# Performance work log

Measured on AMD Instinct MI355X. Metric: run time of the kernel, lower is better.

## Reference

```python
import jax, jax.numpy as jnp
import numpy as np

NEG_INF = -1e9


def setup_inputs() -> dict:
    key = jax.random.key(0)
    k1, k2, k3, k4 = jax.random.split(key, 4)
    B, S, D, P = 4, 256, 512, 256
    sequence = jax.random.normal(k1, (B, S, D), dtype=jnp.float32)
    sequence_mask = jnp.ones((B, S), dtype=jnp.float32)
    W1 = jax.random.normal(k2, (P, D), dtype=jnp.float32) * (1.0 / np.sqrt(D))
    W2 = jax.random.normal(k3, (P, D), dtype=jnp.float32) * (1.0 / np.sqrt(D))
    v = jax.random.normal(k4, (P,), dtype=jnp.float32) * (1.0 / np.sqrt(P))
    return {"sequence": sequence, "sequence_mask": sequence_mask,
            "W1": W1, "W2": W2, "v": v}


def reference(sequence, sequence_mask, W1, W2, v):
    # sequence: [B, S, D]; sequence_mask: [B, S] (1 = valid)
    # Projection (additive) self-attention, vectorized over all query positions.
    pk = jnp.einsum('bsd,pd->bsp', sequence, W1)  # key projections  [B, S, P]
    pq = jnp.einsum('bsd,pd->bsp', sequence, W2)  # query projections [B, S, P]
    # scores[b, i, j] = v . tanh(pq[b, i] + pk[b, j])   (i = query, j = key)
    scores = jnp.einsum('bijp,p->bij',
                        jnp.tanh(pq[:, :, None, :] + pk[:, None, :, :]), v)
    # mask keys, softmax over key dim
    key_mask = sequence_mask[:, None, :] > 0          # [B, 1, S]
    scores = jnp.where(key_mask, scores, NEG_INF)
    weights = jax.nn.softmax(scores, axis=-1)         # [B, Sq, Sk]
    attn = jnp.einsum('bij,bjd->bid', weights, sequence)  # [B, S, D]
    # mask_sequence: zero out invalid query positions
    attn = attn * sequence_mask[:, :, None]
    weights = weights * sequence_mask[:, :, None]
    return attn, weights
```

## Files before the change

kernel.cpp:

```cpp
#include <hip/hip_runtime.h>

constexpr int B = 4;
constexpr int S = 256;
constexpr int D = 512;
constexpr int P = 256;
constexpr float NEG_INF = -1e9f;
constexpr float LOG2E = 1.4426950408889634f;
constexpr float C2 = 2.885390081777927f;

__device__ __forceinline__ float fast_exp2(float x) {
#if __has_builtin(__builtin_amdgcn_exp2f)
    return __builtin_amdgcn_exp2f(x);
#else
    return exp2f(x);
#endif
}

__device__ __forceinline__ float fast_rcp(float x) {
#if __has_builtin(__builtin_amdgcn_rcpf)
    return __builtin_amdgcn_rcpf(x);
#else
    return 1.0f / x;
#endif
}

__global__ __launch_bounds__(256)
void proj_kernel(const float* __restrict__ seq,
                 const float* __restrict__ W1, const float* __restrict__ W2,
                 float* __restrict__ pq, float* __restrict__ pkT) {
    __shared__ float As[64][34];
    __shared__ float Ws[64][68];

    int bid0 = blockIdx.x;
    int bid = (bid0 & 7) * 32 + (bid0 >> 3);

    const float* A;
    const float* Bp;
    float* out;
    if (bid < 128) {
        int mt = bid >> 2, nt = bid & 3;
        A = seq + (size_t)mt * 32 * D;
        Bp = W2 + (size_t)nt * 64 * D;
        out = pq + (size_t)mt * 32 * 256 + nt * 64;
    } else {
        int r = bid - 128;
        int b = r >> 5, t = r & 31;
        int mt = t >> 2, nt = t & 3;
        A = W1 + (size_t)mt * 32 * D;
        Bp = seq + ((size_t)b * S + nt * 64) * D;
        out = pkT + (size_t)b * P * S + (size_t)mt * 32 * 256 + nt * 64;
    }

    int tid = threadIdx.x;
    int tx = tid & 15, ty = tid >> 4;
    int ar = tid >> 3, acg = tid & 7;
    int br = tid >> 2, bcg = tid & 3;
    const float* aptr = A + (size_t)ar * D + acg * 8;
    const float* bptr = Bp + (size_t)br * D + bcg * 16;

    float4 a0, a1, w0, w1, w2, w3;
    a0 = *(const float4*)(aptr);      a1 = *(const float4*)(aptr + 4);
    w0 = *(const float4*)(bptr);      w1 = *(const float4*)(bptr + 4);
    w2 = *(const float4*)(bptr + 8);  w3 = *(const float4*)(bptr + 12);

    float c0[4] = {0.f, 0.f, 0.f, 0.f};
    float c1[4] = {0.f, 0.f, 0.f, 0.f};

    for (int kt = 0; kt < 8; kt++) {
        int ka = acg * 8;
        As[ka + 0][ar] = a0.x; As[ka + 1][ar] = a0.y;
        As[ka + 2][ar] = a0.z; As[ka + 3][ar] = a0.w;
        As[ka + 4][ar] = a1.x; As[ka + 5][ar] = a1.y;
        As[ka + 6][ar] = a1.z; As[ka + 7][ar] = a1.w;
        int kb = bcg * 16;
        Ws[kb + 0][br] = w0.x;  Ws[kb + 1][br] = w0.y;
        Ws[kb + 2][br] = w0.z;  Ws[kb + 3][br] = w0.w;
        Ws[kb + 4][br] = w1.x;  Ws[kb + 5][br] = w1.y;
        Ws[kb + 6][br] = w1.z;  Ws[kb + 7][br] = w1.w;
        Ws[kb + 8][br] = w2.x;  Ws[kb + 9][br] = w2.y;
        Ws[kb + 10][br] = w2.z; Ws[kb + 11][br] = w2.w;
        Ws[kb + 12][br] = w3.x; Ws[kb + 13][br] = w3.y;
        Ws[kb + 14][br] = w3.z; Ws[kb + 15][br] = w3.w;
        __syncthreads();
        if (kt < 7) {
            const float* ap = aptr + (kt + 1) * 64;
            const float* bp = bptr + (kt + 1) * 64;
            a0 = *(const float4*)(ap);     a1 = *(const float4*)(ap + 4);
            w0 = *(const float4*)(bp);     w1 = *(const float4*)(bp + 4);
            w2 = *(const float4*)(bp + 8); w3 = *(const float4*)(bp + 12);
        }
#pragma unroll 8
        for (int k = 0; k < 64; k++) {
            float2 av = *(const float2*)&As[k][ty * 2];
            float4 wv = *(const float4*)&Ws[k][tx * 4];
            c0[0] = fmaf(av.x, wv.x, c0[0]);
            c0[1] = fmaf(av.x, wv.y, c0[1]);
            c0[2] = fmaf(av.x, wv.z, c0[2]);
            c0[3] = fmaf(av.x, wv.w, c0[3]);
            c1[0] = fmaf(av.y, wv.x, c1[0]);
            c1[1] = fmaf(av.y, wv.y, c1[1]);
            c1[2] = fmaf(av.y, wv.z, c1[2]);
            c1[3] = fmaf(av.y, wv.w, c1[3]);
        }
        __syncthreads();
    }
    float4 o0 = {c0[0] * C2, c0[1] * C2, c0[2] * C2, c0[3] * C2};
    float4 o1 = {c1[0] * C2, c1[1] * C2, c1[2] * C2, c1[3] * C2};
    *(float4*)&out[(size_t)(ty * 2 + 0) * 256 + tx * 4] = o0;
    *(float4*)&out[(size_t)(ty * 2 + 1) * 256 + tx * 4] = o1;
}

__global__ __launch_bounds__(512)
void score_attn_kernel(const float* __restrict__ seq,
                       const float* __restrict__ pkT, const float* __restrict__ pq,
                       const float* __restrict__ v, const float* __restrict__ mask,
                       float* __restrict__ wout, float* __restrict__ attn) {
    __shared__ float pqs[2][P];
    __shared__ float vs[P];
    __shared__ float part[4][2][S];
    __shared__ float wsm[S][2];
    __shared__ float p3[4][2][D];
    __shared__ float redm[2][8], reds[2][8];

    int bid0 = blockIdx.x;
    int bid = (bid0 & 7) * 64 + (bid0 >> 3);
    int b = bid >> 7;
    int i0 = (bid & 127) * 2;
    int tid = threadIdx.x;
    int lane = tid & 63, wid = tid >> 6;

    if (tid < 256) {
        ((float2*)pqs)[tid] = ((const float2*)(pq + ((size_t)b * S + i0) * P))[tid];
    } else if (tid < 384) {
        int x = tid - 256;
        float2 vv = ((const float2*)v)[x];
        ((float2*)vs)[x] = make_float2(-2.f * vv.x, -2.f * vv.y);
    }
    __syncthreads();

    {
        int jg = tid & 127, h = tid >> 7;
        const float2* kp = (const float2*)(pkT + (size_t)b * P * S);
        float acc00 = 0.f, acc01 = 0.f, acc10 = 0.f, acc11 = 0.f;
        int pbase = h * 64;
#pragma unroll 4
        for (int pp = 0; pp < 64; pp += 4) {
            int p = pbase + pp;
            float2 k0 = kp[(size_t)(p + 0) * 128 + jg];
            float2 k1 = kp[(size_t)(p + 1) * 128 + jg];
            float2 k2 = kp[(size_t)(p + 2) * 128 + jg];
            float2 k3 = kp[(size_t)(p + 3) * 128 + jg];
            float4 vv = *(const float4*)&vs[p];
            float4 q0 = *(const float4*)&pqs[0][p];
            float4 q1 = *(const float4*)&pqs[1][p];
#define TANH4(kv, vvv, qa, qb)                                     \
            {                                                      \
                float t00 = fast_exp2(kv.x + qa);                  \
                float t01 = fast_exp2(kv.y + qa);                  \
                float t10 = fast_exp2(kv.x + qb);                  \
                float t11 = fast_exp2(kv.y + qb);                  \
                acc00 = fmaf(vvv, fast_rcp(t00 + 1.f), acc00);     \
                acc01 = fmaf(vvv, fast_rcp(t01 + 1.f), acc01);     \
                acc10 = fmaf(vvv, fast_rcp(t10 + 1.f), acc10);     \
                acc11 = fmaf(vvv, fast_rcp(t11 + 1.f), acc11);     \
            }
            TANH4(k0, vv.x, q0.x, q1.x)
            TANH4(k1, vv.y, q0.y, q1.y)
            TANH4(k2, vv.z, q0.z, q1.z)
            TANH4(k3, vv.w, q0.w, q1.w)
#undef TANH4
        }
        int j0 = 2 * jg;
        part[h][0][j0] = acc00; part[h][0][j0 + 1] = acc01;
        part[h][1][j0] = acc10; part[h][1][j0 + 1] = acc11;
    }
    __syncthreads();

    float s0 = -3.0e38f, s1 = -3.0e38f;
    if (tid < 256) {
        int j = tid;
        s0 = (part[0][0][j] + part[1][0][j]) + (part[2][0][j] + part[3][0][j]);
        s1 = (part[0][1][j] + part[1][1][j]) + (part[2][1][j] + part[3][1][j]);
        float km = mask[(size_t)b * S + j];
        if (!(km > 0.f)) { s0 = NEG_INF; s1 = NEG_INF; }
    }
    float m0 = s0, m1 = s1;
#pragma unroll
    for (int off = 32; off >= 1; off >>= 1) {
        m0 = fmaxf(m0, __shfl_xor(m0, off, 64));
        m1 = fmaxf(m1, __shfl_xor(m1, off, 64));
    }
    if (lane == 0) { redm[0][wid] = m0; redm[1][wid] = m1; }
    __syncthreads();
    m0 = fmaxf(fmaxf(redm[0][0], redm[0][1]), fmaxf(redm[0][2], redm[0][3]));
    m1 = fmaxf(fmaxf(redm[1][0], redm[1][1]), fmaxf(redm[1][2], redm[1][3]));
    float e0 = 0.f, e1 = 0.f;
    if (tid < 256) {
        e0 = fast_exp2((s0 - m0) * LOG2E);
        e1 = fast_exp2((s1 - m1) * LOG2E);
    }
    float t0 = e0, t1 = e1;
#pragma unroll
    for (int off = 32; off >= 1; off >>= 1) {
        t0 += __shfl_xor(t0, off, 64);
        t1 += __shfl_xor(t1, off, 64);
    }
    if (lane == 0) { reds[0][wid] = t0; reds[1][wid] = t1; }
    __syncthreads();
    float sum0 = (reds[0][0] + reds[0][1]) + (reds[0][2] + reds[0][3]);
    float sum1 = (reds[1][0] + reds[1][1]) + (reds[1][2] + reds[1][3]);
    if (tid < 256) {
        int j = tid;
        float qm0 = mask[(size_t)b * S + i0];
        float qm1 = mask[(size_t)b * S + i0 + 1];
        float w0 = e0 * fast_rcp(sum0) * qm0;
        float w1 = e1 * fast_rcp(sum1) * qm1;
        wsm[j][0] = w0; wsm[j][1] = w1;
        wout[((size_t)b * S + i0) * S + j] = w0;
        wout[((size_t)b * S + i0 + 1) * S + j] = w1;
    }
    __syncthreads();

    {
        int dg = tid & 127, jh = tid >> 7;
        int d0 = dg * 4;
        const float4* sp = (const float4*)(seq + (size_t)b * S * D);
        float4 A0 = {0.f, 0.f, 0.f, 0.f}, A1 = {0.f, 0.f, 0.f, 0.f};
#pragma unroll 4
        for (int jj = 0; jj < 64; jj++) {
            int j = jh * 64 + jj;
            float4 s4 = sp[(size_t)j * 128 + dg];
            float2 w = *(const float2*)&wsm[j][0];
            A0.x = fmaf(w.x, s4.x, A0.x); A0.y = fmaf(w.x, s4.y, A0.y);
            A0.z = fmaf(w.x, s4.z, A0.z); A0.w = fmaf(w.x, s4.w, A0.w);
            A1.x = fmaf(w.y, s4.x, A1.x); A1.y = fmaf(w.y, s4.y, A1.y);
            A1.z = fmaf(w.y, s4.z, A1.z); A1.w = fmaf(w.y, s4.w, A1.w);
        }
        *(float4*)&p3[jh][0][d0] = A0;
        *(float4*)&p3[jh][1][d0] = A1;
    }
    __syncthreads();
    {
        int d = tid;
        float r0 = (p3[0][0][d] + p3[1][0][d]) + (p3[2][0][d] + p3[3][0][d]);
        float r1 = (p3[0][1][d] + p3[1][1][d]) + (p3[2][1][d] + p3[3][1][d]);
        attn[((size_t)b * S + i0) * D + d] = r0;
        attn[((size_t)b * S + i0 + 1) * D + d] = r1;
    }
}

extern "C" void kernel_launch(void* const* d_in, const int* in_sizes, int n_in,
                              void* d_out, int out_size, void* d_ws, size_t ws_size,
                              hipStream_t stream) {
    const float* seq  = (const float*)d_in[0];
    const float* mask = (const float*)d_in[1];
    const float* W1   = (const float*)d_in[2];
    const float* W2   = (const float*)d_in[3];
    const float* v    = (const float*)d_in[4];

    float* attn = (float*)d_out;
    float* wout = attn + (size_t)B * S * D;

    float* pq  = (float*)d_ws;
    float* pkT = pq + (size_t)B * S * P;

    proj_kernel<<<256, 256, 0, stream>>>(seq, W1, W2, pq, pkT);
    score_attn_kernel<<<B * (S / 2), 512, 0, stream>>>(seq, pkT, pq, v, mask,
                                                       wout, attn);
}
```

Baseline: 44.19 us.

## Precompute exponentials of projections and process four queries per block

The projection kernel now stores exp2 of the scaled projections, so the score loop computes tanh through exp(a+b)=exp(a)*exp(b) with one fma and one reciprocal per pair, with no transcendental inside the quadratic loop. The attention kernel also handles four query rows per block instead of two. This halves the block count and doubles reuse of each loaded key and sequence element. The final weighted sum drops the split-j partial reduction and has each thread loop over all 256 keys for one column. Large projection values could overflow or underflow the exponentials, and the lower block count reduces parallelism.

```diff
diff --git a/kernel.cpp b/kernel.cpp
--- a/kernel.cpp
+++ b/kernel.cpp
@@ -27,7 +27,7 @@
 __global__ __launch_bounds__(256)
 void proj_kernel(const float* __restrict__ seq,
                  const float* __restrict__ W1, const float* __restrict__ W2,
-                 float* __restrict__ pq, float* __restrict__ pkT) {
+                 float* __restrict__ Eq, float* __restrict__ EkT) {
     __shared__ float As[64][34];
     __shared__ float Ws[64][68];
 
@@ -41,14 +41,14 @@
         int mt = bid >> 2, nt = bid & 3;
         A = seq + (size_t)mt * 32 * D;
         Bp = W2 + (size_t)nt * 64 * D;
-        out = pq + (size_t)mt * 32 * 256 + nt * 64;
+        out = Eq + (size_t)mt * 32 * 256 + nt * 64;
     } else {
         int r = bid - 128;
         int b = r >> 5, t = r & 31;
         int mt = t >> 2, nt = t & 3;
         A = W1 + (size_t)mt * 32 * D;
         Bp = seq + ((size_t)b * S + nt * 64) * D;
-        out = pkT + (size_t)b * P * S + (size_t)mt * 32 * 256 + nt * 64;
+        out = EkT + (size_t)b * P * S + (size_t)mt * 32 * 256 + nt * 64;
     }
 
     int tid = threadIdx.x;
@@ -104,148 +104,132 @@
         }
         __syncthreads();
     }
-    float4 o0 = {c0[0] * C2, c0[1] * C2, c0[2] * C2, c0[3] * C2};
-    float4 o1 = {c1[0] * C2, c1[1] * C2, c1[2] * C2, c1[3] * C2};
+    float4 o0 = {fast_exp2(c0[0] * C2), fast_exp2(c0[1] * C2),
+                 fast_exp2(c0[2] * C2), fast_exp2(c0[3] * C2)};
+    float4 o1 = {fast_exp2(c1[0] * C2), fast_exp2(c1[1] * C2),
+                 fast_exp2(c1[2] * C2), fast_exp2(c1[3] * C2)};
     *(float4*)&out[(size_t)(ty * 2 + 0) * 256 + tx * 4] = o0;
     *(float4*)&out[(size_t)(ty * 2 + 1) * 256 + tx * 4] = o1;
 }
 
 __global__ __launch_bounds__(512)
 void score_attn_kernel(const float* __restrict__ seq,
-                       const float* __restrict__ pkT, const float* __restrict__ pq,
+                       const float* __restrict__ EkT, const float* __restrict__ Eq,
                        const float* __restrict__ v, const float* __restrict__ mask,
                        float* __restrict__ wout, float* __restrict__ attn) {
-    __shared__ float pqs[2][P];
+    __shared__ float Eqs[4][P];
     __shared__ float vs[P];
-    __shared__ float part[4][2][S];
-    __shared__ float wsm[S][2];
-    __shared__ float p3[4][2][D];
-    __shared__ float redm[2][8], reds[2][8];
+    __shared__ float part[4][4][S];
+    __shared__ float wsm[S][4];
+    __shared__ float redm[4][8], reds[4][8];
 
     int bid0 = blockIdx.x;
-    int bid = (bid0 & 7) * 64 + (bid0 >> 3);
-    int b = bid >> 7;
-    int i0 = (bid & 127) * 2;
+    int bid = (bid0 & 7) * 32 + (bid0 >> 3);
+    int b = bid >> 6;
+    int i0 = (bid & 63) * 4;
     int tid = threadIdx.x;
     int lane = tid & 63, wid = tid >> 6;
 
-    if (tid < 256) {
-        ((float2*)pqs)[tid] = ((const float2*)(pq + ((size_t)b * S + i0) * P))[tid];
-    } else if (tid < 384) {
-        int x = tid - 256;
-        float2 vv = ((const float2*)v)[x];
-        ((float2*)vs)[x] = make_float2(-2.f * vv.x, -2.f * vv.y);
+    ((float2*)Eqs)[tid] = ((const float2*)(Eq + ((size_t)b * S + i0) * P))[tid];
+    if (tid < 128) {
+        float2 vv = ((const float2*)v)[tid];
+        ((float2*)vs)[tid] = make_float2(-2.f * vv.x, -2.f * vv.y);
     }
     __syncthreads();
 
     {
         int jg = tid & 127, h = tid >> 7;
-        const float2* kp = (const float2*)(pkT + (size_t)b * P * S);
-        float acc00 = 0.f, acc01 = 0.f, acc10 = 0.f, acc11 = 0.f;
+        const float2* kp = (const float2*)(EkT + (size_t)b * P * S) + jg;
         int pbase = h * 64;
-#pragma unroll 4
+        float acc[2][4] = {{0.f, 0.f, 0.f, 0.f}, {0.f, 0.f, 0.f, 0.f}};
         for (int pp = 0; pp < 64; pp += 4) {
             int p = pbase + pp;
-            float2 k0 = kp[(size_t)(p + 0) * 128 + jg];
-            float2 k1 = kp[(size_t)(p + 1) * 128 + jg];
-            float2 k2 = kp[(size_t)(p + 2) * 128 + jg];
-            float2 k3 = kp[(size_t)(p + 3) * 128 + jg];
-            float4 vv = *(const float4*)&vs[p];
-            float4 q0 = *(const float4*)&pqs[0][p];
-            float4 q1 = *(const float4*)&pqs[1][p];
-#define TANH4(kv, vvv, qa, qb)                                     \
-            {                                                      \
-                float t00 = fast_exp2(kv.x + qa);                  \
-                float t01 = fast_exp2(kv.y + qa);                  \
-                float t10 = fast_exp2(kv.x + qb);                  \
-                float t11 = fast_exp2(kv.y + qb);                  \
-                acc00 = fmaf(vvv, fast_rcp(t00 + 1.f), acc00);     \
-                acc01 = fmaf(vvv, fast_rcp(t01 + 1.f), acc01);     \
-                acc10 = fmaf(vvv, fast_rcp(t10 + 1.f), acc10);     \
-                acc11 = fmaf(vvv, fast_rcp(t11 + 1.f), acc11);     \
+            float2 kk[4];
+#pragma unroll
+            for (int t = 0; t < 4; t++) kk[t] = kp[(size_t)(p + t) * 128];
+            float4 vv4 = *(const float4*)&vs[p];
+            float vvv[4] = {vv4.x, vv4.y, vv4.z, vv4.w};
+#pragma unroll
+            for (int q = 0; q < 4; q++) {
+                float4 e4 = *(const float4*)&Eqs[q][p];
+                float ee[4] = {e4.x, e4.y, e4.z, e4.w};
+#pragma unroll
+                for (int t = 0; t < 4; t++) {
+                    float t0 = fmaf(kk[t].x, ee[t], 1.f);
+                    float t1 = fmaf(kk[t].y, ee[t], 1.f);
+                    acc[0][q] = fmaf(vvv[t], fast_rcp(t0), acc[0][q]);
+                    acc[1][q] = fmaf(vvv[t], fast_rcp(t1), acc[1][q]);
+                }
             }
-            TANH4(k0, vv.x, q0.x, q1.x)
-            TANH4(k1, vv.y, q0.y, q1.y)
-            TANH4(k2, vv.z, q0.z, q1.z)
-            TANH4(k3, vv.w, q0.w, q1.w)
-#undef TANH4
-        }
-        int j0 = 2 * jg;
-        part[h][0][j0] = acc00; part[h][0][j0 + 1] = acc01;
-        part[h][1][j0] = acc10; part[h][1][j0 + 1] = acc11;
-    }
-    __syncthreads();
-
-    float s0 = -3.0e38f, s1 = -3.0e38f;
+        }
+#pragma unroll
+        for (int q = 0; q < 4; q++)
+            ((float2*)&part[h][q][0])[jg] = make_float2(acc[0][q], acc[1][q]);
+    }
+    __syncthreads();
+
+    float s[4], e[4] = {0.f, 0.f, 0.f, 0.f};
     if (tid < 256) {
         int j = tid;
-        s0 = (part[0][0][j] + part[1][0][j]) + (part[2][0][j] + part[3][0][j]);
-        s1 = (part[0][1][j] + part[1][1][j]) + (part[2][1][j] + part[3][1][j]);
         float km = mask[(size_t)b * S + j];
-        if (!(km > 0.f)) { s0 = NEG_INF; s1 = NEG_INF; }
-    }
-    float m0 = s0, m1 = s1;
-#pragma unroll
-    for (int off = 32; off >= 1; off >>= 1) {
-        m0 = fmaxf(m0, __shfl_xor(m0, off, 64));
-        m1 = fmaxf(m1, __shfl_xor(m1, off, 64));
-    }
-    if (lane == 0) { redm[0][wid] = m0; redm[1][wid] = m1; }
-    __syncthreads();
-    m0 = fmaxf(fmaxf(redm[0][0], redm[0][1]), fmaxf(redm[0][2], redm[0][3]));
-    m1 = fmaxf(fmaxf(redm[1][0], redm[1][1]), fmaxf(redm[1][2], redm[1][3]));
-    float e0 = 0.f, e1 = 0.f;
+#pragma unroll
+        for (int q = 0; q < 4; q++) {
+            float sv = (part[0][q][j] + part[1][q][j]) +
+                       (part[2][q][j] + part[3][q][j]);
+            s[q] = (km > 0.f) ? sv : NEG_INF;
+            float mm = s[q];
+#pragma unroll
+            for (int off = 32; off >= 1; off >>= 1)
+                mm = fmaxf(mm, __shfl_xor(mm, off, 64));
+            if (lane == 0) redm[q][wid] = mm;
+        }
+    }
+    __syncthreads();
     if (tid < 256) {
-        e0 = fast_exp2((s0 - m0) * LOG2E);
-        e1 = fast_exp2((s1 - m1) * LOG2E);
-    }
-    float t0 = e0, t1 = e1;
-#pragma unroll
-    for (int off = 32; off >= 1; off >>= 1) {
-        t0 += __shfl_xor(t0, off, 64);
-        t1 += __shfl_xor(t1, off, 64);
-    }
-    if (lane == 0) { reds[0][wid] = t0; reds[1][wid] = t1; }
-    __syncthreads();
-    float sum0 = (reds[0][0] + reds[0][1]) + (reds[0][2] + reds[0][3]);
-    float sum1 = (reds[1][0] + reds[1][1]) + (reds[1][2] + reds[1][3]);
+#pragma unroll
+        for (int q = 0; q < 4; q++) {
+            float mm = fmaxf(fmaxf(redm[q][0], redm[q][1]),
+                             fmaxf(redm[q][2], redm[q][3]));
+            float ee = fast_exp2((s[q] - mm) * LOG2E);
+            e[q] = ee;
+            float ss = ee;
+#pragma unroll
+            for (int off = 32; off >= 1; off >>= 1)
+                ss += __shfl_xor(ss, off, 64);
+            if (lane == 0) reds[q][wid] = ss;
+        }
+    }
+    __syncthreads();
     if (tid < 256) {
         int j = tid;
-        float qm0 = mask[(size_t)b * S + i0];
-        float qm1 = mask[(size_t)b * S + i0 + 1];
-        float w0 = e0 * fast_rcp(sum0) * qm0;
-        float w1 = e1 * fast_rcp(sum1) * qm1;
-        wsm[j][0] = w0; wsm[j][1] = w1;
-        wout[((size_t)b * S + i0) * S + j] = w0;
-        wout[((size_t)b * S + i0 + 1) * S + j] = w1;
-    }
-    __syncthreads();
-
-    {
-        int dg = tid & 127, jh = tid >> 7;
-        int d0 = dg * 4;
-        const float4* sp = (const float4*)(seq + (size_t)b * S * D);
-        float4 A0 = {0.f, 0.f, 0.f, 0.f}, A1 = {0.f, 0.f, 0.f, 0.f};
-#pragma unroll 4
-        for (int jj = 0; jj < 64; jj++) {
-            int j = jh * 64 + jj;
-            float4 s4 = sp[(size_t)j * 128 + dg];
-            float2 w = *(const float2*)&wsm[j][0];
-            A0.x = fmaf(w.x, s4.x, A0.x); A0.y = fmaf(w.x, s4.y, A0.y);
-            A0.z = fmaf(w.x, s4.z, A0.z); A0.w = fmaf(w.x, s4.w, A0.w);
-            A1.x = fmaf(w.y, s4.x, A1.x); A1.y = fmaf(w.y, s4.y, A1.y);
-            A1.z = fmaf(w.y, s4.z, A1.z); A1.w = fmaf(w.y, s4.w, A1.w);
-        }
-        *(float4*)&p3[jh][0][d0] = A0;
-        *(float4*)&p3[jh][1][d0] = A1;
-    }
-    __syncthreads();
+#pragma unroll
+        for (int q = 0; q < 4; q++) {
+            float ssum = (reds[q][0] + reds[q][1]) + (reds[q][2] + reds[q][3]);
+            float qm = mask[(size_t)b * S + i0 + q];
+            float w = e[q] * fast_rcp(ssum) * qm;
+            wsm[j][q] = w;
+            wout[((size_t)b * S + i0 + q) * S + j] = w;
+        }
+    }
+    __syncthreads();
+
     {
         int d = tid;
-        float r0 = (p3[0][0][d] + p3[1][0][d]) + (p3[2][0][d] + p3[3][0][d]);
-        float r1 = (p3[0][1][d] + p3[1][1][d]) + (p3[2][1][d] + p3[3][1][d]);
-        attn[((size_t)b * S + i0) * D + d] = r0;
-        attn[((size_t)b * S + i0 + 1) * D + d] = r1;
+        const float* sp = seq + (size_t)b * S * D + d;
+        float a0 = 0.f, a1 = 0.f, a2 = 0.f, a3 = 0.f;
+#pragma unroll 8
+        for (int j = 0; j < S; j++) {
+            float sv = sp[(size_t)j * D];
+            float4 w4 = *(const float4*)&wsm[j][0];
+            a0 = fmaf(w4.x, sv, a0);
+            a1 = fmaf(w4.y, sv, a1);
+            a2 = fmaf(w4.z, sv, a2);
+            a3 = fmaf(w4.w, sv, a3);
+        }
+        attn[((size_t)b * S + i0 + 0) * D + d] = a0;
+        attn[((size_t)b * S + i0 + 1) * D + d] = a1;
+        attn[((size_t)b * S + i0 + 2) * D + d] = a2;
+        attn[((size_t)b * S + i0 + 3) * D + d] = a3;
     }
 }
 
@@ -261,10 +245,10 @@
     float* attn = (float*)d_out;
     float* wout = attn + (size_t)B * S * D;
 
-    float* pq  = (float*)d_ws;
-    float* pkT = pq + (size_t)B * S * P;
-
-    proj_kernel<<<256, 256, 0, stream>>>(seq, W1, W2, pq, pkT);
-    score_attn_kernel<<<B * (S / 2), 512, 0, stream>>>(seq, pkT, pq, v, mask,
+    float* Eq  = (float*)d_ws;
+    float* EkT = Eq + (size_t)B * S * P;
+
+    proj_kernel<<<256, 256, 0, stream>>>(seq, W1, W2, Eq, EkT);
+    score_attn_kernel<<<B * (S / 4), 512, 0, stream>>>(seq, EkT, Eq, v, mask,
                                                        wout, attn);
 }
```

Result: faster. 42.01 us (-4.9%).
